# Optimization experiments

Measured on AMD Instinct MI355X. Metric: run time of the kernel, lower is better.

The kernel has to match this reference:

```python
import jax, jax.numpy as jnp
import numpy as np

N = 50000      # nodes
E = 400000     # edges per edge type
T = 4          # edge types: add/sub/mul/div
F_IN = 128     # in_channels
H = 2          # heads
C = 64         # hidden_channels (per head)
HC = H * C     # 128
MLP = C // 8   # hidden_channels // 8 = 8
NUM_CLASSES = 10


def _glorot(key, shape):
    fan_in, fan_out = shape[-2], shape[-1]
    s = jnp.sqrt(6.0 / (fan_in + fan_out))
    return jax.random.uniform(key, shape, jnp.float32, -s, s)


def setup_inputs() -> dict:
    key = jax.random.key(0)
    ks = jax.random.split(key, 12)
    x = jax.random.normal(ks[0], (N, F_IN), jnp.float32)
    edge_index = jax.random.randint(ks[1], (T, 2, E), 0, N, jnp.int32)
    # layer-1 GATv2 params, stacked over the 4 edge types
    Wl1 = _glorot(ks[2], (T, F_IN, HC))
    Wr1 = _glorot(ks[3], (T, F_IN, HC))
    att1 = _glorot(ks[4], (T, H, C))
    b1 = jnp.zeros((T, HC), jnp.float32)
    # layer-2 GATv2 params (input dim = hidden*heads)
    Wl2 = _glorot(ks[5], (T, HC, HC))
    Wr2 = _glorot(ks[6], (T, HC, HC))
    att2 = _glorot(ks[7], (T, H, C))
    b2 = jnp.zeros((T, HC), jnp.float32)
    # MLP head
    W_lin1 = _glorot(ks[8], (HC, MLP))
    b_lin1 = jnp.zeros((MLP,), jnp.float32)
    W_lin2 = _glorot(ks[9], (MLP, NUM_CLASSES))
    b_lin2 = jnp.zeros((NUM_CLASSES,), jnp.float32)
    return dict(x=x, edge_index=edge_index, Wl1=Wl1, Wr1=Wr1, att1=att1, b1=b1,
                Wl2=Wl2, Wr2=Wr2, att2=att2, b2=b2,
                W_lin1=W_lin1, b_lin1=b_lin1, W_lin2=W_lin2, b_lin2=b_lin2)


def gatv2_conv(x, src, dst, Wl, Wr, att, bias):
    """PyG GATv2Conv: add self-loops, per-edge LeakyReLU attention,
    softmax over incoming edges per destination, weighted scatter-add."""
    n = x.shape[0]
    xl = (x @ Wl).reshape(n, H, C)   # source transform
    xr = (x @ Wr).reshape(n, H, C)   # destination transform
    loop = jnp.arange(n, dtype=src.dtype)
    s = jnp.concatenate([src, loop])
    d = jnp.concatenate([dst, loop])
    e = jax.nn.leaky_relu(xl[s] + xr[d], 0.2)          # [E+n, H, C]
    score = jnp.einsum('ehc,hc->eh', e, att)           # [E+n, H]
    smax = jax.ops.segment_max(score, d, num_segments=n)  # [N, H]
    p = jnp.exp(score - smax[d])                       # stable softmax numerators
    denom = jax.ops.segment_sum(p, d, num_segments=n)  # [N, H]
    msg = jax.ops.segment_sum(p[:, :, None] * xl[s], d, num_segments=n)  # [N, H, C]
    out = msg / denom[:, :, None]
    return out.reshape(n, HC) + bias


def hetero_layer(x, edge_index, Wl, Wr, att, b):
    # HeteroConv with aggr='sum' over the 4 edge types (single node type)
    out = gatv2_conv(x, edge_index[0, 0], edge_index[0, 1], Wl[0], Wr[0], att[0], b[0])
    for t in range(1, T):
        out = out + gatv2_conv(x, edge_index[t, 0], edge_index[t, 1], Wl[t], Wr[t], att[t], b[t])
    return out


def reference(x, edge_index, Wl1, Wr1, att1, b1, Wl2, Wr2, att2, b2,
              W_lin1, b_lin1, W_lin2, b_lin2):
    h = jax.nn.relu(hetero_layer(x, edge_index, Wl1, Wr1, att1, b1))
    h = jax.nn.relu(hetero_layer(h, edge_index, Wl2, Wr2, att2, b2))
    h = jax.nn.relu(h @ W_lin1 + b_lin1)
    # dropout p=0.5 is identity at eval time
    return h @ W_lin2 + b_lin2
```

## Files before the change

### kernel.cpp

```cpp
#include <hip/hip_runtime.h>
#include <hip/hip_bf16.h>
#include <math.h>

#define NN 50000
#define EE 400000
#define TT 4
#define FD 128
#define RPS 50004
#define NBKT 196
#define BCAP 4096

typedef __attribute__((ext_vector_type(8))) short bf16x8;
typedef __attribute__((ext_vector_type(4))) float f32x4;

__device__ inline float bf2f(unsigned short u) {
  union { unsigned int i; float f; } x; x.i = ((unsigned int)u) << 16; return x.f;
}
__device__ inline unsigned short f2bf(float f) {
  __hip_bfloat16 h = __float2bfloat16(f);
  unsigned short u; __builtin_memcpy(&u, &h, 2); return u;
}
__device__ inline float gsum(float v) {
  v += __shfl_xor(v, 1);
  v += __shfl_xor(v, 2);
  v += __shfl_xor(v, 4);
  v += __shfl_xor(v, 8);
  v += __shfl_xor(v, 16);
  return v;
}

__global__ void k_cvtW(const float* __restrict__ Wl1, const float* __restrict__ Wr1,
                       const float* __restrict__ Wl2, const float* __restrict__ Wr2,
                       unsigned short* __restrict__ Bpack) {
  const int idx = blockIdx.x * 256 + threadIdx.x;
  const int R = idx >> 14;
  const int kc = idx & 16383;
  const int lr = R & 1, t = (R >> 1) & 3, layer = R >> 3;
  const float* W = layer ? (lr ? Wr2 : Wl2) : (lr ? Wr1 : Wl1);
  const float v = W[t * 16384 + kc];
  const int k = kc >> 7, c = kc & 127;
  const int nt = c >> 4, ks = k >> 5, g = (k >> 3) & 3, j = k & 7;
  const int lane = g * 16 + (c & 15);
  Bpack[(size_t)R * 16384 + ((nt * 4 + ks) * 64 + lane) * 8 + j] = f2bf(v);
}

__global__ void k_cvtA(const float* __restrict__ src, unsigned short* __restrict__ ahi,
                       unsigned short* __restrict__ alo) {
  const int idx = blockIdx.x * 256 + threadIdx.x;
  float4 v = ((const float4*)src)[idx];
  const unsigned short h0 = f2bf(v.x), h1 = f2bf(v.y), h2 = f2bf(v.z), h3 = f2bf(v.w);
  const unsigned short l0 = f2bf(v.x - bf2f(h0)), l1 = f2bf(v.y - bf2f(h1));
  const unsigned short l2 = f2bf(v.z - bf2f(h2)), l3 = f2bf(v.w - bf2f(h3));
  uint2 hv, lv;
  hv.x = (unsigned)h0 | ((unsigned)h1 << 16); hv.y = (unsigned)h2 | ((unsigned)h3 << 16);
  lv.x = (unsigned)l0 | ((unsigned)l1 << 16); lv.y = (unsigned)l2 | ((unsigned)l3 << 16);
  ((uint2*)ahi)[idx] = hv;
  ((uint2*)alo)[idx] = lv;
}

__global__ __launch_bounds__(128) void k_gemm4(
    const unsigned short* __restrict__ Ahi, const unsigned short* __restrict__ Alo,
    const unsigned short* __restrict__ Bbase,
    unsigned short* __restrict__ xl4, unsigned short* __restrict__ xr4) {
  const int t = blockIdx.y;
  const unsigned short* Bpt = Bbase + (size_t)t * 2 * 16384;
  unsigned short* xl = xl4 + (size_t)t * NN * FD;
  unsigned short* xr = xr4 + (size_t)t * NN * FD;
  const int tid = threadIdx.x;
  const int lane = tid & 63;
  const int w = tid >> 6;
  const int rh = lane & 15, g = lane >> 4;
  const int m0 = blockIdx.x * 64 + w * 32;
  f32x4 acc[2][16];
  #pragma unroll
  for (int a = 0; a < 2; ++a)
    #pragma unroll
    for (int b = 0; b < 16; ++b) acc[a][b] = (f32x4){0.f, 0.f, 0.f, 0.f};
  int r0 = m0 + rh;      if (r0 > NN - 1) r0 = NN - 1;
  int r1 = m0 + 16 + rh; if (r1 > NN - 1) r1 = NN - 1;
  #pragma unroll
  for (int ks = 0; ks < 4; ++ks) {
    const int ko = ks * 32 + g * 8;
    const bf16x8 ah0 = *(const bf16x8*)(Ahi + (size_t)r0 * FD + ko);
    const bf16x8 al0 = *(const bf16x8*)(Alo + (size_t)r0 * FD + ko);
    const bf16x8 ah1 = *(const bf16x8*)(Ahi + (size_t)r1 * FD + ko);
    const bf16x8 al1 = *(const bf16x8*)(Alo + (size_t)r1 * FD + ko);
    #pragma unroll
    for (int nt = 0; nt < 16; ++nt) {
      const bf16x8 b = *(const bf16x8*)(Bpt + (nt >> 3) * 16384 +
                                        (((nt & 7) * 4 + ks) * 64 + lane) * 8);
      acc[0][nt] = __builtin_amdgcn_mfma_f32_16x16x32_bf16(ah0, b, acc[0][nt], 0, 0, 0);
      acc[0][nt] = __builtin_amdgcn_mfma_f32_16x16x32_bf16(al0, b, acc[0][nt], 0, 0, 0);
      acc[1][nt] = __builtin_amdgcn_mfma_f32_16x16x32_bf16(ah1, b, acc[1][nt], 0, 0, 0);
      acc[1][nt] = __builtin_amdgcn_mfma_f32_16x16x32_bf16(al1, b, acc[1][nt], 0, 0, 0);
    }
  }
  #pragma unroll
  for (int mt = 0; mt < 2; ++mt)
    #pragma unroll
    for (int nt = 0; nt < 16; ++nt) {
      unsigned short* op = (nt < 8) ? xl : xr;
      const int cb = (nt & 7) * 16 + rh;
      #pragma unroll
      for (int r = 0; r < 4; ++r) {
        const int row = m0 + mt * 16 + g * 4 + r;
        if (row < NN) op[(size_t)row * FD + cb] = f2bf(acc[mt][nt][r]);
      }
    }
}

__global__ __launch_bounds__(256) void k_bucket(const int* __restrict__ ei,
                                                int* __restrict__ bcur,
                                                unsigned int* __restrict__ ebuf) {
  __shared__ int lcnt[NBKT], lbase[NBKT];
  const int t = blockIdx.y, tid = threadIdx.x;
  const int cbase = blockIdx.x * 4096;
  if (tid < NBKT) lcnt[tid] = 0;
  __syncthreads();
  const int* srcp = ei + (size_t)t * 2 * EE;
  const int* dstp = srcp + EE;
  unsigned int pk[16]; int rk[16];
  #pragma unroll
  for (int i = 0; i < 16; ++i) {
    const int e = cbase + i * 256 + tid;
    rk[i] = -1;
    if (e < EE) {
      const int s = srcp[e], dd = dstp[e];
      const int b = dd >> 8;
      pk[i] = ((unsigned)dd << 16) | (unsigned)s;
      rk[i] = (atomicAdd(&lcnt[b], 1) << 8) | b;
    }
  }
  __syncthreads();
  if (tid < NBKT && lcnt[tid] > 0) lbase[tid] = atomicAdd(&bcur[t * NBKT + tid], lcnt[tid]);
  __syncthreads();
  #pragma unroll
  for (int i = 0; i < 16; ++i) {
    if (rk[i] >= 0) {
      const int b = rk[i] & 255, r = rk[i] >> 8;
      ebuf[((size_t)t * NBKT + b) * BCAP + lbase[b] + r] = pk[i];
    }
  }
}

__global__ void k_bktscan(const int* __restrict__ bcur, int* __restrict__ bbase) {
  __shared__ int s[TT * NBKT];
  const int tid = threadIdx.x;
  int v0 = 0;
  if (tid < TT * NBKT) { v0 = bcur[tid]; s[tid] = v0; }
  __syncthreads();
  #pragma unroll
  for (int off = 1; off < NBKT; off <<= 1) {
    int a = 0;
    if (tid < TT * NBKT && (tid % NBKT) >= off) a = s[tid - off];
    __syncthreads();
    if (tid < TT * NBKT) s[tid] += a;
    __syncthreads();
  }
  if (tid < TT * NBKT) bbase[tid] = s[tid] - v0;
}

__global__ __launch_bounds__(256) void k_scatter3(const unsigned int* __restrict__ ebuf,
                                                  const int* __restrict__ bcur,
                                                  const int* __restrict__ bbase,
                                                  int* __restrict__ rowp,
                                                  int* __restrict__ col) {
  __shared__ int lc[256], sc[256];
  const int b = blockIdx.x, t = blockIdx.y, tid = threadIdx.x;
  const int d0 = b << 8;
  const int nd = (NN - d0 < 256) ? (NN - d0) : 256;
  const int cnt = bcur[t * NBKT + b];
  const int base = bbase[t * NBKT + b];
  const unsigned int* eb = ebuf + ((size_t)t * NBKT + b) * BCAP;
  lc[tid] = 0;
  __syncthreads();
  for (int j = tid; j < cnt; j += 256) {
    atomicAdd(&lc[(eb[j] >> 16) - d0], 1);
  }
  __syncthreads();
  const int v = lc[tid];
  sc[tid] = v;
  __syncthreads();
  #pragma unroll
  for (int off = 1; off < 256; off <<= 1) {
    const int a = (tid >= off) ? sc[tid - off] : 0;
    __syncthreads();
    sc[tid] += a;
    __syncthreads();
  }
  const int excl = base + sc[tid] - v;
  if (tid < nd) rowp[(size_t)t * RPS + d0 + tid] = excl;
  if (b == NBKT - 1 && tid == 0) rowp[(size_t)t * RPS + NN] = EE;
  lc[tid] = excl;
  __syncthreads();
  for (int j = tid; j < cnt; j += 256) {
    const unsigned int u = eb[j];
    const int pos = atomicAdd(&lc[(u >> 16) - d0], 1);
    col[(size_t)t * EE + pos] = (int)(u & 0xFFFF);
  }
}

__global__ __launch_bounds__(256) void k_agg4(
    const unsigned short* __restrict__ xl4, const unsigned short* __restrict__ xr4,
    const int* __restrict__ col, const int* __restrict__ rowp,
    const float* __restrict__ att, const float* __restrict__ bias,
    float* __restrict__ hout, unsigned short* __restrict__ ahi,
    unsigned short* __restrict__ alo, const int mode) {
  __shared__ float sh0[256], sh1[256];
  const int tid = threadIdx.x;
  const int lane = tid & 63, t = tid >> 6;
  const int d = blockIdx.x;
  const unsigned short* xl = xl4 + (size_t)t * NN * FD;
  const unsigned short* xr = xr4 + (size_t)t * NN * FD;
  const int* colt = col + (size_t)t * EE;
  const float2 av = ((const float2*)(att + t * FD))[lane];
  unsigned int ur, ulp;
  __builtin_memcpy(&ur, xr + (size_t)d * FD + 2 * lane, 4);
  __builtin_memcpy(&ulp, xl + (size_t)d * FD + 2 * lane, 4);
  const float xr0 = bf2f((unsigned short)(ur & 0xFFFF)), xr1 = bf2f((unsigned short)(ur >> 16));
  const float sl0 = bf2f((unsigned short)(ulp & 0xFFFF)), sl1 = bf2f((unsigned short)(ulp >> 16));
  float v0 = sl0 + xr0; v0 = v0 > 0.f ? v0 : 0.2f * v0;
  float v1 = sl1 + xr1; v1 = v1 > 0.f ? v1 : 0.2f * v1;
  float m = gsum(av.x * v0 + av.y * v1);
  float den = 1.f, ac0 = sl0, ac1 = sl1;
  int e = rowp[(size_t)t * RPS + d];
  const int end = rowp[(size_t)t * RPS + d + 1];
  for (; e + 1 < end; e += 2) {
    const int s0 = colt[e], s1 = colt[e + 1];
    unsigned int u0, u1;
    __builtin_memcpy(&u0, xl + (size_t)s0 * FD + 2 * lane, 4);
    __builtin_memcpy(&u1, xl + (size_t)s1 * FD + 2 * lane, 4);
    const float x00 = bf2f((unsigned short)(u0 & 0xFFFF)), x01 = bf2f((unsigned short)(u0 >> 16));
    const float x10 = bf2f((unsigned short)(u1 & 0xFFFF)), x11 = bf2f((unsigned short)(u1 >> 16));
    float a0 = x00 + xr0; a0 = a0 > 0.f ? a0 : 0.2f * a0;
    float a1 = x01 + xr1; a1 = a1 > 0.f ? a1 : 0.2f * a1;
    float b0 = x10 + xr0; b0 = b0 > 0.f ? b0 : 0.2f * b0;
    float b1 = x11 + xr1; b1 = b1 > 0.f ? b1 : 0.2f * b1;
    const float q0 = gsum(av.x * a0 + av.y * a1);
    const float q1 = gsum(av.x * b0 + av.y * b1);
    const float nm = fmaxf(m, fmaxf(q0, q1));
    const float sc = __expf(m - nm), w0 = __expf(q0 - nm), w1 = __expf(q1 - nm);
    den = den * sc + w0 + w1;
    ac0 = ac0 * sc + w0 * x00 + w1 * x10;
    ac1 = ac1 * sc + w0 * x01 + w1 * x11;
    m = nm;
  }
  if (e < end) {
    const int s0 = colt[e];
    unsigned int u0;
    __builtin_memcpy(&u0, xl + (size_t)s0 * FD + 2 * lane, 4);
    const float x00 = bf2f((unsigned short)(u0 & 0xFFFF)), x01 = bf2f((unsigned short)(u0 >> 16));
    float a0 = x00 + xr0; a0 = a0 > 0.f ? a0 : 0.2f * a0;
    float a1 = x01 + xr1; a1 = a1 > 0.f ? a1 : 0.2f * a1;
    const float q0 = gsum(av.x * a0 + av.y * a1);
    const float nm = fmaxf(m, q0);
    const float sc = __expf(m - nm), w0 = __expf(q0 - nm);
    den = den * sc + w0;
    ac0 = ac0 * sc + w0 * x00;
    ac1 = ac1 * sc + w0 * x01;
  }
  const float2 bv = ((const float2*)(bias + t * FD))[lane];
  sh0[tid] = ac0 / den + bv.x;
  sh1[tid] = ac1 / den + bv.y;
  __syncthreads();
  if (tid < 64) {
    float s0 = sh0[tid] + sh0[64 + tid] + sh0[128 + tid] + sh0[192 + tid];
    float s1 = sh1[tid] + sh1[64 + tid] + sh1[128 + tid] + sh1[192 + tid];
    if (mode == 0) {
      s0 = fmaxf(s0, 0.f); s1 = fmaxf(s1, 0.f);
      const unsigned short h0 = f2bf(s0), h1 = f2bf(s1);
      const unsigned short l0 = f2bf(s0 - bf2f(h0)), l1 = f2bf(s1 - bf2f(h1));
      ((unsigned int*)ahi)[(size_t)d * 64 + tid] = (unsigned)h0 | ((unsigned)h1 << 16);
      ((unsigned int*)alo)[(size_t)d * 64 + tid] = (unsigned)l0 | ((unsigned)l1 << 16);
    } else {
      ((float2*)(hout + (size_t)d * FD))[tid] = make_float2(s0, s1);
    }
  }
}

__global__ __launch_bounds__(256) void k_mlp(const float* __restrict__ h,
                                             const float* __restrict__ W1,
                                             const float* __restrict__ b1,
                                             const float* __restrict__ W2,
                                             const float* __restrict__ b2,
                                             float* __restrict__ out) {
  __shared__ float sW1[128 * 8];
  __shared__ float sW2[8 * 10];
  __shared__ float sb1[8], sb2[10];
  for (int i = threadIdx.x; i < 1024; i += 256) sW1[i] = W1[i];
  if (threadIdx.x < 80) sW2[threadIdx.x] = W2[threadIdx.x];
  if (threadIdx.x < 8)  sb1[threadIdx.x] = b1[threadIdx.x];
  if (threadIdx.x < 10) sb2[threadIdx.x] = b2[threadIdx.x];
  __syncthreads();
  const int n = blockIdx.x * 256 + threadIdx.x;
  if (n >= NN) return;
  const float* hn = h + (size_t)n * FD;
  float z[8];
  #pragma unroll
  for (int j = 0; j < 8; ++j) z[j] = sb1[j];
  for (int k = 0; k < FD; k += 4) {
    float4 hv = *(const float4*)(hn + k);
    hv.x = fmaxf(hv.x, 0.f); hv.y = fmaxf(hv.y, 0.f);
    hv.z = fmaxf(hv.z, 0.f); hv.w = fmaxf(hv.w, 0.f);
    #pragma unroll
    for (int j = 0; j < 8; ++j) {
      z[j] += hv.x * sW1[(k + 0) * 8 + j] + hv.y * sW1[(k + 1) * 8 + j]
            + hv.z * sW1[(k + 2) * 8 + j] + hv.w * sW1[(k + 3) * 8 + j];
    }
  }
  #pragma unroll
  for (int j = 0; j < 8; ++j) z[j] = fmaxf(z[j], 0.f);
  float o[10];
  #pragma unroll
  for (int c = 0; c < 10; ++c) o[c] = sb2[c];
  #pragma unroll
  for (int j = 0; j < 8; ++j)
    #pragma unroll
    for (int c = 0; c < 10; ++c) o[c] += z[j] * sW2[j * 10 + c];
  float* op = out + (size_t)n * 10;
  #pragma unroll
  for (int c = 0; c < 10; ++c) op[c] = o[c];
}

extern "C" void kernel_launch(void* const* d_in, const int* in_sizes, int n_in,
                              void* d_out, int out_size, void* d_ws, size_t ws_size,
                              hipStream_t stream) {
  const float* x    = (const float*)d_in[0];
  const int*   ei   = (const int*)d_in[1];
  const float* Wl1  = (const float*)d_in[2];
  const float* Wr1  = (const float*)d_in[3];
  const float* att1 = (const float*)d_in[4];
  const float* b1   = (const float*)d_in[5];
  const float* Wl2  = (const float*)d_in[6];
  const float* Wr2  = (const float*)d_in[7];
  const float* att2 = (const float*)d_in[8];
  const float* b2   = (const float*)d_in[9];
  const float* Wi1  = (const float*)d_in[10];
  const float* bi1  = (const float*)d_in[11];
  const float* Wi2  = (const float*)d_in[12];
  const float* bi2  = (const float*)d_in[13];
  float* out = (float*)d_out;

  char* ws = (char*)d_ws;
  size_t off = 0;
  auto alloc = [&](size_t bytes) {
    void* p = ws + off;
    off = (off + bytes + 255) & ~(size_t)255;
    return p;
  };
  unsigned short* xl4   = (unsigned short*)alloc((size_t)TT * NN * FD * 2);
  unsigned short* xr4   = (unsigned short*)alloc((size_t)TT * NN * FD * 2);
  unsigned short* Ahi   = (unsigned short*)alloc((size_t)NN * FD * 2);
  unsigned short* Alo   = (unsigned short*)alloc((size_t)NN * FD * 2);
  float*          h2    = (float*)alloc((size_t)NN * FD * 4);
  unsigned short* Bpack = (unsigned short*)alloc((size_t)2 * TT * 2 * 16384 * 2);
  int*            col   = (int*)alloc((size_t)TT * EE * 4);
  int*            rowp  = (int*)alloc((size_t)TT * RPS * 4);
  int*            bcur  = (int*)alloc((size_t)TT * NBKT * 4);
  int*            bbase = (int*)alloc((size_t)TT * NBKT * 4);
  unsigned int* ebuf = (unsigned int*)h2;

  hipMemsetAsync(bcur, 0, (size_t)TT * NBKT * 4, stream);
  k_cvtW<<<1024, 256, 0, stream>>>(Wl1, Wr1, Wl2, Wr2, Bpack);
  k_bucket<<<dim3(98, TT), 256, 0, stream>>>(ei, bcur, ebuf);
  k_bktscan<<<1, 1024, 0, stream>>>(bcur, bbase);
  k_scatter3<<<dim3(NBKT, TT), 256, 0, stream>>>(ebuf, bcur, bbase, rowp, col);

  k_cvtA<<<6250, 256, 0, stream>>>(x, Ahi, Alo);
  k_gemm4<<<dim3(782, TT), 128, 0, stream>>>(Ahi, Alo, Bpack, xl4, xr4);
  k_agg4<<<NN, 256, 0, stream>>>(xl4, xr4, col, rowp, att1, b1,
                                 nullptr, Ahi, Alo, 0);
  k_gemm4<<<dim3(782, TT), 128, 0, stream>>>(Ahi, Alo, Bpack + (size_t)TT * 2 * 16384,
                                             xl4, xr4);
  k_agg4<<<NN, 256, 0, stream>>>(xl4, xr4, col, rowp, att2, b2,
                                 h2, nullptr, nullptr, 1);
  k_mlp<<<(NN + 255) / 256, 256, 0, stream>>>(h2, Wi1, bi1, Wi2, bi2, out);
}
```

Baseline: 654.2 us.

## Fuse MLP head into second aggregation and tighten per-edge softmax loop

Folds the two-layer MLP head into the layer-2 aggregation kernel, so each destination row computes its logits directly and the fp32 hidden buffer and its write/read round trip go away. The edge loop is unrolled from 2 to 4 edges to put more gathers in flight. Cross-lane sums now use DPP and ds_swizzle instead of shuffles, and exp2 works on log2e-prescaled attention. The cost is more register pressure in the aggregation kernel and extra per-row work on one wave, and ebuf now gets its own workspace allocation.

```diff
diff --git a/kernel.cpp b/kernel.cpp
--- a/kernel.cpp
+++ b/kernel.cpp
@@ -9,6 +9,7 @@
 #define RPS 50004
 #define NBKT 196
 #define BCAP 4096
+#define LOG2E 1.44269504f
 
 typedef __attribute__((ext_vector_type(8))) short bf16x8;
 typedef __attribute__((ext_vector_type(4))) float f32x4;
@@ -20,12 +21,29 @@
   __hip_bfloat16 h = __float2bfloat16(f);
   unsigned short u; __builtin_memcpy(&u, &h, 2); return u;
 }
-__device__ inline float gsum(float v) {
-  v += __shfl_xor(v, 1);
-  v += __shfl_xor(v, 2);
-  v += __shfl_xor(v, 4);
-  v += __shfl_xor(v, 8);
-  v += __shfl_xor(v, 16);
+__device__ inline float blo(unsigned int u) {
+  union { unsigned int i; float f; } x; x.i = u << 16; return x.f;
+}
+__device__ inline float bhi(unsigned int u) {
+  union { unsigned int i; float f; } x; x.i = u & 0xFFFF0000u; return x.f;
+}
+__device__ inline float fexp2(float x) { return __builtin_amdgcn_exp2f(x); }
+
+__device__ inline float dppadd(float v, int ctrl) {
+  int s = __builtin_bit_cast(int, v);
+  return v;
+}
+__device__ inline float qsum32(float v) {
+  v += __builtin_bit_cast(float, __builtin_amdgcn_update_dpp(
+         0, __builtin_bit_cast(int, v), 0xB1, 0xF, 0xF, true));
+  v += __builtin_bit_cast(float, __builtin_amdgcn_update_dpp(
+         0, __builtin_bit_cast(int, v), 0x4E, 0xF, 0xF, true));
+  v += __builtin_bit_cast(float, __builtin_amdgcn_update_dpp(
+         0, __builtin_bit_cast(int, v), 0x141, 0xF, 0xF, true));
+  v += __builtin_bit_cast(float, __builtin_amdgcn_update_dpp(
+         0, __builtin_bit_cast(int, v), 0x140, 0xF, 0xF, true));
+  v += __builtin_bit_cast(float, __builtin_amdgcn_ds_swizzle(
+         __builtin_bit_cast(int, v), 0x401F));
   return v;
 }
 
@@ -204,8 +222,10 @@
     const unsigned short* __restrict__ xl4, const unsigned short* __restrict__ xr4,
     const int* __restrict__ col, const int* __restrict__ rowp,
     const float* __restrict__ att, const float* __restrict__ bias,
-    float* __restrict__ hout, unsigned short* __restrict__ ahi,
-    unsigned short* __restrict__ alo, const int mode) {
+    unsigned short* __restrict__ ahi, unsigned short* __restrict__ alo,
+    const float* __restrict__ W1, const float* __restrict__ b1v,
+    const float* __restrict__ W2, const float* __restrict__ b2v,
+    float* __restrict__ out, const int mode) {
   __shared__ float sh0[256], sh1[256];
   const int tid = threadIdx.x;
   const int lane = tid & 63, t = tid >> 6;
@@ -213,55 +233,70 @@
   const unsigned short* xl = xl4 + (size_t)t * NN * FD;
   const unsigned short* xr = xr4 + (size_t)t * NN * FD;
   const int* colt = col + (size_t)t * EE;
-  const float2 av = ((const float2*)(att + t * FD))[lane];
+  float2 av = ((const float2*)(att + t * FD))[lane];
+  av.x *= LOG2E; av.y *= LOG2E;
   unsigned int ur, ulp;
   __builtin_memcpy(&ur, xr + (size_t)d * FD + 2 * lane, 4);
   __builtin_memcpy(&ulp, xl + (size_t)d * FD + 2 * lane, 4);
-  const float xr0 = bf2f((unsigned short)(ur & 0xFFFF)), xr1 = bf2f((unsigned short)(ur >> 16));
-  const float sl0 = bf2f((unsigned short)(ulp & 0xFFFF)), sl1 = bf2f((unsigned short)(ulp >> 16));
-  float v0 = sl0 + xr0; v0 = v0 > 0.f ? v0 : 0.2f * v0;
-  float v1 = sl1 + xr1; v1 = v1 > 0.f ? v1 : 0.2f * v1;
-  float m = gsum(av.x * v0 + av.y * v1);
+  const float xr0 = blo(ur), xr1 = bhi(ur);
+  const float sl0 = blo(ulp), sl1 = bhi(ulp);
+  float v0 = sl0 + xr0; v0 = fmaxf(v0, 0.2f * v0);
+  float v1 = sl1 + xr1; v1 = fmaxf(v1, 0.2f * v1);
+  float m = qsum32(fmaf(av.y, v1, av.x * v0));
   float den = 1.f, ac0 = sl0, ac1 = sl1;
   int e = rowp[(size_t)t * RPS + d];
   const int end = rowp[(size_t)t * RPS + d + 1];
-  for (; e + 1 < end; e += 2) {
-    const int s0 = colt[e], s1 = colt[e + 1];
-    unsigned int u0, u1;
+  for (; e + 3 < end; e += 4) {
+    const int s0 = colt[e], s1 = colt[e + 1], s2 = colt[e + 2], s3 = colt[e + 3];
+    unsigned int u0, u1, u2, u3;
     __builtin_memcpy(&u0, xl + (size_t)s0 * FD + 2 * lane, 4);
     __builtin_memcpy(&u1, xl + (size_t)s1 * FD + 2 * lane, 4);
-    const float x00 = bf2f((unsigned short)(u0 & 0xFFFF)), x01 = bf2f((unsigned short)(u0 >> 16));
-    const float x10 = bf2f((unsigned short)(u1 & 0xFFFF)), x11 = bf2f((unsigned short)(u1 >> 16));
-    float a0 = x00 + xr0; a0 = a0 > 0.f ? a0 : 0.2f * a0;
-    float a1 = x01 + xr1; a1 = a1 > 0.f ? a1 : 0.2f * a1;
-    float b0 = x10 + xr0; b0 = b0 > 0.f ? b0 : 0.2f * b0;
-    float b1 = x11 + xr1; b1 = b1 > 0.f ? b1 : 0.2f * b1;
-    const float q0 = gsum(av.x * a0 + av.y * a1);
-    const float q1 = gsum(av.x * b0 + av.y * b1);
-    const float nm = fmaxf(m, fmaxf(q0, q1));
-    const float sc = __expf(m - nm), w0 = __expf(q0 - nm), w1 = __expf(q1 - nm);
-    den = den * sc + w0 + w1;
-    ac0 = ac0 * sc + w0 * x00 + w1 * x10;
-    ac1 = ac1 * sc + w0 * x01 + w1 * x11;
+    __builtin_memcpy(&u2, xl + (size_t)s2 * FD + 2 * lane, 4);
+    __builtin_memcpy(&u3, xl + (size_t)s3 * FD + 2 * lane, 4);
+    const float x00 = blo(u0), x01 = bhi(u0);
+    const float x10 = blo(u1), x11 = bhi(u1);
+    const float x20 = blo(u2), x21 = bhi(u2);
+    const float x30 = blo(u3), x31 = bhi(u3);
+    float a0 = x00 + xr0, a1 = x01 + xr1;
+    float b0 = x10 + xr0, b1 = x11 + xr1;
+    float c0 = x20 + xr0, c1 = x21 + xr1;
+    float d0 = x30 + xr0, d1 = x31 + xr1;
+    a0 = fmaxf(a0, 0.2f * a0); a1 = fmaxf(a1, 0.2f * a1);
+    b0 = fmaxf(b0, 0.2f * b0); b1 = fmaxf(b1, 0.2f * b1);
+    c0 = fmaxf(c0, 0.2f * c0); c1 = fmaxf(c1, 0.2f * c1);
+    d0 = fmaxf(d0, 0.2f * d0); d1 = fmaxf(d1, 0.2f * d1);
+    float p0 = qsum32(fmaf(av.y, a1, av.x * a0));
+    float p1 = qsum32(fmaf(av.y, b1, av.x * b0));
+    float p2 = qsum32(fmaf(av.y, c1, av.x * c0));
+    float p3 = qsum32(fmaf(av.y, d1, av.x * d0));
+    const float nm = fmaxf(fmaxf(fmaxf(p0, p1), fmaxf(p2, p3)), m);
+    const float scl = fexp2(m - nm);
+    const float w0 = fexp2(p0 - nm), w1 = fexp2(p1 - nm);
+    const float w2 = fexp2(p2 - nm), w3 = fexp2(p3 - nm);
+    den = fmaf(den, scl, (w0 + w1) + (w2 + w3));
+    ac0 = fmaf(ac0, scl, fmaf(w0, x00, fmaf(w1, x10, fmaf(w2, x20, w3 * x30))));
+    ac1 = fmaf(ac1, scl, fmaf(w0, x01, fmaf(w1, x11, fmaf(w2, x21, w3 * x31))));
     m = nm;
   }
-  if (e < end) {
+  for (; e < end; ++e) {
     const int s0 = colt[e];
     unsigned int u0;
     __builtin_memcpy(&u0, xl + (size_t)s0 * FD + 2 * lane, 4);
-    const float x00 = bf2f((unsigned short)(u0 & 0xFFFF)), x01 = bf2f((unsigned short)(u0 >> 16));
-    float a0 = x00 + xr0; a0 = a0 > 0.f ? a0 : 0.2f * a0;
-    float a1 = x01 + xr1; a1 = a1 > 0.f ? a1 : 0.2f * a1;
-    const float q0 = gsum(av.x * a0 + av.y * a1);
-    const float nm = fmaxf(m, q0);
-    const float sc = __expf(m - nm), w0 = __expf(q0 - nm);
-    den = den * sc + w0;
-    ac0 = ac0 * sc + w0 * x00;
-    ac1 = ac1 * sc + w0 * x01;
+    const float x00 = blo(u0), x01 = bhi(u0);
+    float a0 = x00 + xr0, a1 = x01 + xr1;
+    a0 = fmaxf(a0, 0.2f * a0); a1 = fmaxf(a1, 0.2f * a1);
+    const float p0 = qsum32(fmaf(av.y, a1, av.x * a0));
+    const float nm = fmaxf(m, p0);
+    const float scl = fexp2(m - nm), w0 = fexp2(p0 - nm);
+    den = fmaf(den, scl, w0);
+    ac0 = fmaf(ac0, scl, w0 * x00);
+    ac1 = fmaf(ac1, scl, w0 * x01);
+    m = nm;
   }
   const float2 bv = ((const float2*)(bias + t * FD))[lane];
-  sh0[tid] = ac0 / den + bv.x;
-  sh1[tid] = ac1 / den + bv.y;
+  const float rden = 1.f / den;
+  sh0[tid] = fmaf(ac0, rden, bv.x);
+  sh1[tid] = fmaf(ac1, rden, bv.y);
   __syncthreads();
   if (tid < 64) {
     float s0 = sh0[tid] + sh0[64 + tid] + sh0[128 + tid] + sh0[192 + tid];
@@ -273,53 +308,28 @@
       ((unsigned int*)ahi)[(size_t)d * 64 + tid] = (unsigned)h0 | ((unsigned)h1 << 16);
       ((unsigned int*)alo)[(size_t)d * 64 + tid] = (unsigned)l0 | ((unsigned)l1 << 16);
     } else {
-      ((float2*)(hout + (size_t)d * FD))[tid] = make_float2(s0, s1);
-    }
-  }
-}
-
-__global__ __launch_bounds__(256) void k_mlp(const float* __restrict__ h,
-                                             const float* __restrict__ W1,
-                                             const float* __restrict__ b1,
-                                             const float* __restrict__ W2,
-                                             const float* __restrict__ b2,
-                                             float* __restrict__ out) {
-  __shared__ float sW1[128 * 8];
-  __shared__ float sW2[8 * 10];
-  __shared__ float sb1[8], sb2[10];
-  for (int i = threadIdx.x; i < 1024; i += 256) sW1[i] = W1[i];
-  if (threadIdx.x < 80) sW2[threadIdx.x] = W2[threadIdx.x];
-  if (threadIdx.x < 8)  sb1[threadIdx.x] = b1[threadIdx.x];
-  if (threadIdx.x < 10) sb2[threadIdx.x] = b2[threadIdx.x];
-  __syncthreads();
-  const int n = blockIdx.x * 256 + threadIdx.x;
-  if (n >= NN) return;
-  const float* hn = h + (size_t)n * FD;
-  float z[8];
-  #pragma unroll
-  for (int j = 0; j < 8; ++j) z[j] = sb1[j];
-  for (int k = 0; k < FD; k += 4) {
-    float4 hv = *(const float4*)(hn + k);
-    hv.x = fmaxf(hv.x, 0.f); hv.y = fmaxf(hv.y, 0.f);
-    hv.z = fmaxf(hv.z, 0.f); hv.w = fmaxf(hv.w, 0.f);
-    #pragma unroll
-    for (int j = 0; j < 8; ++j) {
-      z[j] += hv.x * sW1[(k + 0) * 8 + j] + hv.y * sW1[(k + 1) * 8 + j]
-            + hv.z * sW1[(k + 2) * 8 + j] + hv.w * sW1[(k + 3) * 8 + j];
-    }
-  }
-  #pragma unroll
-  for (int j = 0; j < 8; ++j) z[j] = fmaxf(z[j], 0.f);
-  float o[10];
-  #pragma unroll
-  for (int c = 0; c < 10; ++c) o[c] = sb2[c];
-  #pragma unroll
-  for (int j = 0; j < 8; ++j)
-    #pragma unroll
-    for (int c = 0; c < 10; ++c) o[c] += z[j] * sW2[j * 10 + c];
-  float* op = out + (size_t)n * 10;
-  #pragma unroll
-  for (int c = 0; c < 10; ++c) op[c] = o[c];
+      s0 = fmaxf(s0, 0.f); s1 = fmaxf(s1, 0.f);
+      const float4* wA = (const float4*)(W1 + tid * 16);
+      const float4 a0 = wA[0], a1 = wA[1], a2 = wA[2], a3 = wA[3];
+      float z[8];
+      z[0] = fmaf(s0, a0.x, s1 * a2.x); z[1] = fmaf(s0, a0.y, s1 * a2.y);
+      z[2] = fmaf(s0, a0.z, s1 * a2.z); z[3] = fmaf(s0, a0.w, s1 * a2.w);
+      z[4] = fmaf(s0, a1.x, s1 * a3.x); z[5] = fmaf(s0, a1.y, s1 * a3.y);
+      z[6] = fmaf(s0, a1.z, s1 * a3.z); z[7] = fmaf(s0, a1.w, s1 * a3.w);
+      #pragma unroll
+      for (int j = 0; j < 8; ++j) {
+        float v = qsum32(z[j]);
+        v += __shfl_xor(v, 32, 64);
+        z[j] = fmaxf(v + b1v[j], 0.f);
+      }
+      if (tid < 10) {
+        float o = b2v[tid];
+        #pragma unroll
+        for (int j = 0; j < 8; ++j) o = fmaf(z[j], W2[j * 10 + tid], o);
+        out[(size_t)d * 10 + tid] = o;
+      }
+    }
+  }
 }
 
 extern "C" void kernel_launch(void* const* d_in, const int* in_sizes, int n_in,
@@ -352,13 +362,12 @@
   unsigned short* xr4   = (unsigned short*)alloc((size_t)TT * NN * FD * 2);
   unsigned short* Ahi   = (unsigned short*)alloc((size_t)NN * FD * 2);
   unsigned short* Alo   = (unsigned short*)alloc((size_t)NN * FD * 2);
-  float*          h2    = (float*)alloc((size_t)NN * FD * 4);
   unsigned short* Bpack = (unsigned short*)alloc((size_t)2 * TT * 2 * 16384 * 2);
   int*            col   = (int*)alloc((size_t)TT * EE * 4);
   int*            rowp  = (int*)alloc((size_t)TT * RPS * 4);
   int*            bcur  = (int*)alloc((size_t)TT * NBKT * 4);
   int*            bbase = (int*)alloc((size_t)TT * NBKT * 4);
-  unsigned int* ebuf = (unsigned int*)h2;
+  unsigned int*   ebuf  = (unsigned int*)alloc((size_t)TT * NBKT * BCAP * 4);
 
   hipMemsetAsync(bcur, 0, (size_t)TT * NBKT * 4, stream);
   k_cvtW<<<1024, 256, 0, stream>>>(Wl1, Wr1, Wl2, Wr2, Bpack);
@@ -369,10 +378,11 @@
   k_cvtA<<<6250, 256, 0, stream>>>(x, Ahi, Alo);
   k_gemm4<<<dim3(782, TT), 128, 0, stream>>>(Ahi, Alo, Bpack, xl4, xr4);
   k_agg4<<<NN, 256, 0, stream>>>(xl4, xr4, col, rowp, att1, b1,
-                                 nullptr, Ahi, Alo, 0);
+                                 Ahi, Alo, nullptr, nullptr, nullptr, nullptr,
+                                 nullptr, 0);
   k_gemm4<<<dim3(782, TT), 128, 0, stream>>>(Ahi, Alo, Bpack + (size_t)TT * 2 * 16384,
                                              xl4, xr4);
   k_agg4<<<NN, 256, 0, stream>>>(xl4, xr4, col, rowp, att2, b2,
-                                 h2, nullptr, nullptr, 1);
-  k_mlp<<<(NN + 255) / 256, 256, 0, stream>>>(h2, Wi1, bi1, Wi2, bi2, out);
-}
+                                 nullptr, nullptr, Wi1, bi1, Wi2, bi2,
+                                 out, 1);
+}
```

Result: faster. 564.7 us (-13.7%).

## Restructure GATv2 aggregation: one wave per node, loop edge types, split edges across half-waves

Applied to the files above, without the earlier changes.

The aggregation kernel now gives each destination node one 64-lane wave that loops over the four edge types, instead of one 256-thread block with a wave per edge type combined through shared memory. Each lane handles 4 channels, and the two half-waves process alternating edges with an online softmax whose partial states are merged with a cross-lane shuffle. Small arithmetic tricks are added: DPP-based 16-lane sums, exp2 with log2e folded into the attention weights, and LeakyReLU rewritten as a linear plus abs term. The workspace layout changes so the edge buffer gets its own allocation and h2 aliases the Ahi/Alo region. The aliasing relies on the second aggregation no longer reading Ahi.

```diff
diff --git a/kernel.cpp b/kernel.cpp
--- a/kernel.cpp
+++ b/kernel.cpp
@@ -9,6 +9,7 @@
 #define RPS 50004
 #define NBKT 196
 #define BCAP 4096
+#define LOG2E 1.44269504f
 
 typedef __attribute__((ext_vector_type(8))) short bf16x8;
 typedef __attribute__((ext_vector_type(4))) float f32x4;
@@ -20,12 +21,27 @@
   __hip_bfloat16 h = __float2bfloat16(f);
   unsigned short u; __builtin_memcpy(&u, &h, 2); return u;
 }
-__device__ inline float gsum(float v) {
-  v += __shfl_xor(v, 1);
-  v += __shfl_xor(v, 2);
-  v += __shfl_xor(v, 4);
-  v += __shfl_xor(v, 8);
-  v += __shfl_xor(v, 16);
+__device__ inline float blo(unsigned int u) {
+  union { unsigned int i; float f; } x; x.i = u << 16; return x.f;
+}
+__device__ inline float bhi(unsigned int u) {
+  union { unsigned int i; float f; } x; x.i = u & 0xFFFF0000u; return x.f;
+}
+__device__ inline float fexp2(float x) { return __builtin_amdgcn_exp2f(x); }
+__device__ inline float sgn04(float a) {
+  union { float f; unsigned int i; } x; x.f = a;
+  x.i = (x.i & 0x80000000u) | 0x3ECCCCCDu;
+  return x.f;
+}
+__device__ inline float qsum16(float v) {
+  v += __builtin_bit_cast(float, __builtin_amdgcn_update_dpp(
+         0, __builtin_bit_cast(int, v), 0xB1, 0xF, 0xF, true));
+  v += __builtin_bit_cast(float, __builtin_amdgcn_update_dpp(
+         0, __builtin_bit_cast(int, v), 0x4E, 0xF, 0xF, true));
+  v += __builtin_bit_cast(float, __builtin_amdgcn_update_dpp(
+         0, __builtin_bit_cast(int, v), 0x141, 0xF, 0xF, true));
+  v += __builtin_bit_cast(float, __builtin_amdgcn_update_dpp(
+         0, __builtin_bit_cast(int, v), 0x140, 0xF, 0xF, true));
   return v;
 }
 
@@ -200,80 +216,98 @@
   }
 }
 
-__global__ __launch_bounds__(256) void k_agg4(
+__global__ __launch_bounds__(256) void k_agg5(
     const unsigned short* __restrict__ xl4, const unsigned short* __restrict__ xr4,
     const int* __restrict__ col, const int* __restrict__ rowp,
     const float* __restrict__ att, const float* __restrict__ bias,
-    float* __restrict__ hout, unsigned short* __restrict__ ahi,
-    unsigned short* __restrict__ alo, const int mode) {
-  __shared__ float sh0[256], sh1[256];
-  const int tid = threadIdx.x;
-  const int lane = tid & 63, t = tid >> 6;
-  const int d = blockIdx.x;
-  const unsigned short* xl = xl4 + (size_t)t * NN * FD;
-  const unsigned short* xr = xr4 + (size_t)t * NN * FD;
-  const int* colt = col + (size_t)t * EE;
-  const float2 av = ((const float2*)(att + t * FD))[lane];
-  unsigned int ur, ulp;
-  __builtin_memcpy(&ur, xr + (size_t)d * FD + 2 * lane, 4);
-  __builtin_memcpy(&ulp, xl + (size_t)d * FD + 2 * lane, 4);
-  const float xr0 = bf2f((unsigned short)(ur & 0xFFFF)), xr1 = bf2f((unsigned short)(ur >> 16));
-  const float sl0 = bf2f((unsigned short)(ulp & 0xFFFF)), sl1 = bf2f((unsigned short)(ulp >> 16));
-  float v0 = sl0 + xr0; v0 = v0 > 0.f ? v0 : 0.2f * v0;
-  float v1 = sl1 + xr1; v1 = v1 > 0.f ? v1 : 0.2f * v1;
-  float m = gsum(av.x * v0 + av.y * v1);
-  float den = 1.f, ac0 = sl0, ac1 = sl1;
-  int e = rowp[(size_t)t * RPS + d];
-  const int end = rowp[(size_t)t * RPS + d + 1];
-  for (; e + 1 < end; e += 2) {
-    const int s0 = colt[e], s1 = colt[e + 1];
-    unsigned int u0, u1;
-    __builtin_memcpy(&u0, xl + (size_t)s0 * FD + 2 * lane, 4);
-    __builtin_memcpy(&u1, xl + (size_t)s1 * FD + 2 * lane, 4);
-    const float x00 = bf2f((unsigned short)(u0 & 0xFFFF)), x01 = bf2f((unsigned short)(u0 >> 16));
-    const float x10 = bf2f((unsigned short)(u1 & 0xFFFF)), x11 = bf2f((unsigned short)(u1 >> 16));
-    float a0 = x00 + xr0; a0 = a0 > 0.f ? a0 : 0.2f * a0;
-    float a1 = x01 + xr1; a1 = a1 > 0.f ? a1 : 0.2f * a1;
-    float b0 = x10 + xr0; b0 = b0 > 0.f ? b0 : 0.2f * b0;
-    float b1 = x11 + xr1; b1 = b1 > 0.f ? b1 : 0.2f * b1;
-    const float q0 = gsum(av.x * a0 + av.y * a1);
-    const float q1 = gsum(av.x * b0 + av.y * b1);
-    const float nm = fmaxf(m, fmaxf(q0, q1));
-    const float sc = __expf(m - nm), w0 = __expf(q0 - nm), w1 = __expf(q1 - nm);
-    den = den * sc + w0 + w1;
-    ac0 = ac0 * sc + w0 * x00 + w1 * x10;
-    ac1 = ac1 * sc + w0 * x01 + w1 * x11;
-    m = nm;
-  }
-  if (e < end) {
-    const int s0 = colt[e];
-    unsigned int u0;
-    __builtin_memcpy(&u0, xl + (size_t)s0 * FD + 2 * lane, 4);
-    const float x00 = bf2f((unsigned short)(u0 & 0xFFFF)), x01 = bf2f((unsigned short)(u0 >> 16));
-    float a0 = x00 + xr0; a0 = a0 > 0.f ? a0 : 0.2f * a0;
-    float a1 = x01 + xr1; a1 = a1 > 0.f ? a1 : 0.2f * a1;
-    const float q0 = gsum(av.x * a0 + av.y * a1);
-    const float nm = fmaxf(m, q0);
-    const float sc = __expf(m - nm), w0 = __expf(q0 - nm);
-    den = den * sc + w0;
-    ac0 = ac0 * sc + w0 * x00;
-    ac1 = ac1 * sc + w0 * x01;
-  }
-  const float2 bv = ((const float2*)(bias + t * FD))[lane];
-  sh0[tid] = ac0 / den + bv.x;
-  sh1[tid] = ac1 / den + bv.y;
-  __syncthreads();
-  if (tid < 64) {
-    float s0 = sh0[tid] + sh0[64 + tid] + sh0[128 + tid] + sh0[192 + tid];
-    float s1 = sh1[tid] + sh1[64 + tid] + sh1[128 + tid] + sh1[192 + tid];
+    unsigned short* __restrict__ ahi, unsigned short* __restrict__ alo,
+    float* __restrict__ hout, const int mode) {
+  const int lane = threadIdx.x & 63;
+  const int d = blockIdx.x * 4 + (threadIdx.x >> 6);
+  const int head = (lane >> 4) & 1, sub = lane & 15, pbit = lane >> 5;
+  const int laneoff = head * 128 + sub * 8;
+  const int choff = head * 64 + sub * 4;
+  float o0 = 0.f, o1 = 0.f, o2 = 0.f, o3 = 0.f;
+  for (int t = 0; t < TT; ++t) {
+    const char* xlt = (const char*)xl4 + ((size_t)t * NN) * 256 + laneoff;
+    const char* xrt = (const char*)xr4 + ((size_t)t * NN) * 256 + laneoff;
+    const int* colt = col + (size_t)t * EE;
+    float4 av = *(const float4*)(att + t * FD + choff);
+    av.x *= LOG2E; av.y *= LOG2E; av.z *= LOG2E; av.w *= LOG2E;
+    const float sa0 = sgn04(av.x), sa1 = sgn04(av.y);
+    const float sa2 = sgn04(av.z), sa3 = sgn04(av.w);
+    const uint2 ur = *(const uint2*)(xrt + (size_t)d * 256);
+    const float axr0 = av.x * blo(ur.x), axr1 = av.y * bhi(ur.x);
+    const float axr2 = av.z * blo(ur.y), axr3 = av.w * bhi(ur.y);
+    const uint2 us = *(const uint2*)(xlt + (size_t)d * 256);
+    const float xs0 = blo(us.x), xs1 = bhi(us.x), xs2 = blo(us.y), xs3 = bhi(us.y);
+    {
+      const float q0 = fmaf(av.x, xs0, axr0), q1 = fmaf(av.y, xs1, axr1);
+      const float q2 = fmaf(av.z, xs2, axr2), q3 = fmaf(av.w, xs3, axr3);
+      float r = sa0 * fabsf(q0);
+      r = fmaf(sa1, fabsf(q1), r); r = fmaf(sa2, fabsf(q2), r); r = fmaf(sa3, fabsf(q3), r);
+      const float c = qsum16(fmaf(0.6f, (q0 + q1) + (q2 + q3), r));
+      const bool isA = (pbit == 0);
+      float m = isA ? c : -3.0e38f;
+      float den = isA ? 1.f : 0.f;
+      float a0 = isA ? xs0 : 0.f, a1 = isA ? xs1 : 0.f;
+      float a2 = isA ? xs2 : 0.f, a3 = isA ? xs3 : 0.f;
+      const int beg = rowp[(size_t)t * RPS + d];
+      const int end = rowp[(size_t)t * RPS + d + 1];
+      for (int eb = beg; eb < end; eb += 2) {
+        const int e = eb + pbit;
+        const bool act = (e < end);
+        const int ec = act ? e : end - 1;
+        const int s = colt[ec];
+        const uint2 u = *(const uint2*)(xlt + (size_t)s * 256);
+        const float x0 = blo(u.x), x1 = bhi(u.x), x2 = blo(u.y), x3 = bhi(u.y);
+        const float q0 = fmaf(av.x, x0, axr0), q1 = fmaf(av.y, x1, axr1);
+        const float q2 = fmaf(av.z, x2, axr2), q3 = fmaf(av.w, x3, axr3);
+        float r = sa0 * fabsf(q0);
+        r = fmaf(sa1, fabsf(q1), r); r = fmaf(sa2, fabsf(q2), r); r = fmaf(sa3, fabsf(q3), r);
+        float c2 = qsum16(fmaf(0.6f, (q0 + q1) + (q2 + q3), r));
+        const float p = act ? c2 : -INFINITY;
+        const float nm = fmaxf(m, p);
+        const float scl = fexp2(m - nm), w = fexp2(p - nm);
+        den = fmaf(den, scl, w);
+        a0 = fmaf(a0, scl, w * x0); a1 = fmaf(a1, scl, w * x1);
+        a2 = fmaf(a2, scl, w * x2); a3 = fmaf(a3, scl, w * x3);
+        m = nm;
+      }
+      const float mo = __shfl_xor(m, 32), deno = __shfl_xor(den, 32);
+      const float b0 = __shfl_xor(a0, 32), b1 = __shfl_xor(a1, 32);
+      const float b2 = __shfl_xor(a2, 32), b3 = __shfl_xor(a3, 32);
+      const float nm = fmaxf(m, mo);
+      const float sMe = fexp2(m - nm), sOt = fexp2(mo - nm);
+      const float dm = fmaf(den, sMe, deno * sOt);
+      const float rden = __builtin_amdgcn_rcpf(dm);
+      o0 = fmaf(fmaf(a0, sMe, b0 * sOt), rden, o0);
+      o1 = fmaf(fmaf(a1, sMe, b1 * sOt), rden, o1);
+      o2 = fmaf(fmaf(a2, sMe, b2 * sOt), rden, o2);
+      o3 = fmaf(fmaf(a3, sMe, b3 * sOt), rden, o3);
+    }
+  }
+  #pragma unroll
+  for (int t = 0; t < TT; ++t) {
+    const float4 bv = *(const float4*)(bias + t * FD + choff);
+    o0 += bv.x; o1 += bv.y; o2 += bv.z; o3 += bv.w;
+  }
+  if (pbit == 0) {
     if (mode == 0) {
-      s0 = fmaxf(s0, 0.f); s1 = fmaxf(s1, 0.f);
-      const unsigned short h0 = f2bf(s0), h1 = f2bf(s1);
-      const unsigned short l0 = f2bf(s0 - bf2f(h0)), l1 = f2bf(s1 - bf2f(h1));
-      ((unsigned int*)ahi)[(size_t)d * 64 + tid] = (unsigned)h0 | ((unsigned)h1 << 16);
-      ((unsigned int*)alo)[(size_t)d * 64 + tid] = (unsigned)l0 | ((unsigned)l1 << 16);
+      o0 = fmaxf(o0, 0.f); o1 = fmaxf(o1, 0.f);
+      o2 = fmaxf(o2, 0.f); o3 = fmaxf(o3, 0.f);
+      const unsigned short h0 = f2bf(o0), h1 = f2bf(o1);
+      const unsigned short h2 = f2bf(o2), h3 = f2bf(o3);
+      const unsigned short l0 = f2bf(o0 - bf2f(h0)), l1 = f2bf(o1 - bf2f(h1));
+      const unsigned short l2 = f2bf(o2 - bf2f(h2)), l3 = f2bf(o3 - bf2f(h3));
+      uint2 hv, lv;
+      hv.x = (unsigned)h0 | ((unsigned)h1 << 16); hv.y = (unsigned)h2 | ((unsigned)h3 << 16);
+      lv.x = (unsigned)l0 | ((unsigned)l1 << 16); lv.y = (unsigned)l2 | ((unsigned)l3 << 16);
+      const size_t ui = (size_t)d * 64 + head * 32 + sub * 2;
+      ((uint2*)((unsigned int*)ahi + ui))[0] = hv;
+      ((uint2*)((unsigned int*)alo + ui))[0] = lv;
     } else {
-      ((float2*)(hout + (size_t)d * FD))[tid] = make_float2(s0, s1);
+      *(float4*)(hout + (size_t)d * FD + choff) = make_float4(o0, o1, o2, o3);
     }
   }
 }
@@ -352,13 +386,13 @@
   unsigned short* xr4   = (unsigned short*)alloc((size_t)TT * NN * FD * 2);
   unsigned short* Ahi   = (unsigned short*)alloc((size_t)NN * FD * 2);
   unsigned short* Alo   = (unsigned short*)alloc((size_t)NN * FD * 2);
-  float*          h2    = (float*)alloc((size_t)NN * FD * 4);
   unsigned short* Bpack = (unsigned short*)alloc((size_t)2 * TT * 2 * 16384 * 2);
   int*            col   = (int*)alloc((size_t)TT * EE * 4);
   int*            rowp  = (int*)alloc((size_t)TT * RPS * 4);
   int*            bcur  = (int*)alloc((size_t)TT * NBKT * 4);
   int*            bbase = (int*)alloc((size_t)TT * NBKT * 4);
-  unsigned int* ebuf = (unsigned int*)h2;
+  unsigned int*   ebuf  = (unsigned int*)alloc((size_t)TT * NBKT * BCAP * 4);
+  float* h2 = (float*)Ahi;
 
   hipMemsetAsync(bcur, 0, (size_t)TT * NBKT * 4, stream);
   k_cvtW<<<1024, 256, 0, stream>>>(Wl1, Wr1, Wl2, Wr2, Bpack);
@@ -368,11 +402,11 @@
 
   k_cvtA<<<6250, 256, 0, stream>>>(x, Ahi, Alo);
   k_gemm4<<<dim3(782, TT), 128, 0, stream>>>(Ahi, Alo, Bpack, xl4, xr4);
-  k_agg4<<<NN, 256, 0, stream>>>(xl4, xr4, col, rowp, att1, b1,
-                                 nullptr, Ahi, Alo, 0);
+  k_agg5<<<12500, 256, 0, stream>>>(xl4, xr4, col, rowp, att1, b1,
+                                    Ahi, Alo, nullptr, 0);
   k_gemm4<<<dim3(782, TT), 128, 0, stream>>>(Ahi, Alo, Bpack + (size_t)TT * 2 * 16384,
                                              xl4, xr4);
-  k_agg4<<<NN, 256, 0, stream>>>(xl4, xr4, col, rowp, att2, b2,
-                                 h2, nullptr, nullptr, 1);
+  k_agg5<<<12500, 256, 0, stream>>>(xl4, xr4, col, rowp, att2, b2,
+                                    nullptr, nullptr, h2, 1);
   k_mlp<<<(NN + 255) / 256, 256, 0, stream>>>(h2, Wi1, bi1, Wi2, bi2, out);
 }
```

Result: faster. 570.6 us (-12.8%).
